# Kernel optimization log

Measured on AMD Instinct MI355X. Metric: run time of the kernel, lower is better.

Reference implementation:

```python
import jax, jax.numpy as jnp
import numpy as np

B, S, E = 4, 2048, 512
Q, FFN = 8, 2048


def setup_inputs() -> dict:
    key = jax.random.key(0)
    k_x, k_th, k_w1, k_w2 = jax.random.split(key, 4)
    x = jax.random.normal(k_x, (B, S, E), dtype=jnp.float32)
    # trainable RY angles, one per wire
    theta = jax.random.normal(k_th, (Q,), dtype=jnp.float32)
    W1 = jax.random.normal(k_w1, (Q, FFN), dtype=jnp.float32) / np.sqrt(Q)
    b1 = jnp.zeros((FFN,), dtype=jnp.float32)
    W2 = jax.random.normal(k_w2, (FFN, E), dtype=jnp.float32) / np.sqrt(FFN)
    b2 = jnp.zeros((E,), dtype=jnp.float32)
    return {"x": x, "theta": theta, "W1": W1, "b1": b1, "W2": W2, "b2": b2}


def reference(x, theta, W1, b1, W2, b2):
    # Quantum circuit: |0> -> RX(x_i) -> RY(theta_i) -> <Z> per wire.
    # No entangling gates, so the 8-qubit state factorizes; simulate each
    # qubit's 2 complex amplitudes, batched over all tokens & wires at once.
    n_wires = theta.shape[0]
    xq = x[..., :n_wires]                     # encoder uses input_idx 0..7: [B,S,Q]
    # RX(x)|0> = cos(x/2)|0> - i sin(x/2)|1>
    a = jnp.cos(xq * 0.5).astype(jnp.complex64)
    b = (-1j) * jnp.sin(xq * 0.5).astype(jnp.complex64)
    # RY(theta) = [[c,-s],[s,c]], c=cos(theta/2), s=sin(theta/2)
    c = jnp.cos(theta * 0.5).astype(jnp.complex64)
    s = jnp.sin(theta * 0.5).astype(jnp.complex64)
    a2 = c * a - s * b
    b2_ = s * a + c * b
    # <Z> = |amp0|^2 - |amp1|^2  -> [B,S,Q]
    z = (jnp.abs(a2) ** 2 - jnp.abs(b2_) ** 2).astype(x.dtype)
    # dropout is identity at inference
    h = jax.nn.relu(jnp.einsum('bsq,qf->bsf', z, W1) + b1)
    return jnp.einsum('bsf,fe->bse', h, W2) + b2
```

## Files before the change

### kernel.cpp

```cpp
#include <hip/hip_runtime.h>
#include <hip/hip_bf16.h>

typedef __bf16 bf16_t;
typedef __bf16 bf16x4 __attribute__((ext_vector_type(4)));
typedef __bf16 bf16x8 __attribute__((ext_vector_type(8)));
typedef float f32x4 __attribute__((ext_vector_type(4)));

#define M_TOT 8192
#define N_TOT 512
#define K_TOT 2048
#define E_TOT 512

typedef const __attribute__((address_space(1))) void* gas_ptr;
typedef __attribute__((address_space(3))) void* las_ptr;

__device__ __forceinline__ void gload_lds16(const void* g, void* l) {
    __builtin_amdgcn_global_load_lds((gas_ptr)g, (las_ptr)l, 16, 0, 0);
}

__device__ __forceinline__ bf16x8 zero8() {
    bf16x8 v;
#pragma unroll
    for (int i = 0; i < 8; ++i) v[i] = (bf16_t)0.0f;
    return v;
}

__global__ __launch_bounds__(256)
void prep3_kernel(const float* __restrict__ x,
                  const float* __restrict__ theta,
                  const float* __restrict__ W1,
                  const float* __restrict__ b1,
                  const float* __restrict__ W2,
                  bf16_t* __restrict__ W2t,
                  bf16_t* __restrict__ zb,
                  bf16_t* __restrict__ W1t)
{
    const int b = blockIdx.x;
    if (b < 256) {
        __shared__ bf16_t T[64][66];
        const int k0 = (b >> 3) * 64;
        const int n0 = (b & 7) * 64;
        const int kl = threadIdx.x >> 4;
        const int n4 = threadIdx.x & 15;
#pragma unroll
        for (int i = 0; i < 4; ++i) {
            int k = kl + i * 16;
            float4 v = *(const float4*)(W2 + (size_t)(k0 + k) * N_TOT + n0 + n4 * 4);
            T[n4 * 4 + 0][k] = (bf16_t)v.x;
            T[n4 * 4 + 1][k] = (bf16_t)v.y;
            T[n4 * 4 + 2][k] = (bf16_t)v.z;
            T[n4 * 4 + 3][k] = (bf16_t)v.w;
        }
        __syncthreads();
        const int nl = threadIdx.x >> 4;
        const int k4 = threadIdx.x & 15;
#pragma unroll
        for (int i = 0; i < 4; ++i) {
            int n = nl + i * 16;
            bf16x4 v;
            v[0] = T[n][k4 * 4 + 0];
            v[1] = T[n][k4 * 4 + 1];
            v[2] = T[n][k4 * 4 + 2];
            v[3] = T[n][k4 * 4 + 3];
            *(bf16x4*)(W2t + (size_t)(n0 + n) * K_TOT + k0 + k4 * 4) = v;
        }
    } else if (b < 288) {
        const int m = (b - 256) * 256 + threadIdx.x;
        float4 x0 = *(const float4*)(x + (size_t)m * E_TOT);
        float4 x1 = *(const float4*)(x + (size_t)m * E_TOT + 4);
        float xs[8] = {x0.x, x0.y, x0.z, x0.w, x1.x, x1.y, x1.z, x1.w};
        bf16x8 lo;
#pragma unroll
        for (int q = 0; q < 8; ++q)
            lo[q] = (bf16_t)(__builtin_cosf(theta[q]) * __builtin_cosf(xs[q]));
        bf16x8 hi = zero8();
        hi[0] = (bf16_t)1.0f;
        *(bf16x8*)(zb + (size_t)m * 16)     = lo;
        *(bf16x8*)(zb + (size_t)m * 16 + 8) = hi;
    } else {
        const int f = (b - 288) * 256 + threadIdx.x;
        bf16x8 lo;
#pragma unroll
        for (int q = 0; q < 8; ++q)
            lo[q] = (bf16_t)W1[(size_t)q * K_TOT + f];
        bf16x8 hi = zero8();
        hi[0] = (bf16_t)b1[f];
        *(bf16x8*)(W1t + (size_t)f * 16)     = lo;
        *(bf16x8*)(W1t + (size_t)f * 16 + 8) = hi;
    }
}

__global__ __launch_bounds__(256, 2)
void ffq_gemm_kernel(const bf16_t* __restrict__ zb,
                     const bf16_t* __restrict__ W1t,
                     const bf16_t* __restrict__ W2t,
                     const float* __restrict__ b2,
                     float* __restrict__ out)
{
    __shared__ bf16_t Alds[64 * 64];
    __shared__ bf16_t Blds[128 * 64];

    const int t = threadIdx.x;
    const int w = t >> 6, l = t & 63;
    const int m_base = blockIdx.y * 64;
    const int n_base = blockIdx.x * 128;
    const int wm = w >> 1, wn = w & 1;
    const int l15 = l & 15, lq = l >> 4;
    const int lrow = l >> 3, lseg = l & 7;

    bf16x8 zfrag = zero8();
    if (lq < 2)
        zfrag = *(const bf16x8*)(zb + (size_t)(m_base + w * 16 + l15) * 16 + lq * 8);

    f32x4 acc[2][4];
#pragma unroll
    for (int mt = 0; mt < 2; ++mt)
#pragma unroll
        for (int nt = 0; nt < 4; ++nt)
            acc[mt][nt] = (f32x4){0.f, 0.f, 0.f, 0.f};

    for (int k0 = 0; k0 < K_TOT; k0 += 64) {
        bf16x8 wf[4];
#pragma unroll
        for (int ft = 0; ft < 4; ++ft) wf[ft] = zero8();
        if (lq < 2) {
#pragma unroll
            for (int ft = 0; ft < 4; ++ft)
                wf[ft] = *(const bf16x8*)(W1t + (size_t)(k0 + ft * 16 + l15) * 16 + lq * 8);
        }

#pragma unroll
        for (int j = 0; j < 4; ++j) {
            int n = j * 32 + w * 8 + lrow;
            int g = lseg ^ (n & 7);
            gload_lds16(W2t + (size_t)(n_base + n) * K_TOT + k0 + g * 8,
                        (bf16_t*)Blds + j * 2048 + w * 512);
        }

        const int m_loc = w * 16 + l15;
#pragma unroll
        for (int ft = 0; ft < 4; ++ft) {
            f32x4 hacc = (f32x4){0.f, 0.f, 0.f, 0.f};
            hacc = __builtin_amdgcn_mfma_f32_16x16x32_bf16(wf[ft], zfrag, hacc, 0, 0, 0);
            bf16x4 hv;
#pragma unroll
            for (int r = 0; r < 4; ++r) hv[r] = (bf16_t)fmaxf(hacc[r], 0.f);
            int fseg = ft * 2 + (lq >> 1);
            int slot = fseg ^ (m_loc & 7);
            *(bf16x4*)(Alds + m_loc * 64 + slot * 8 + (lq & 1) * 4) = hv;
        }

        __syncthreads();

#pragma unroll
        for (int kk = 0; kk < 2; ++kk) {
            bf16x8 af[2], bfr[4];
#pragma unroll
            for (int mt = 0; mt < 2; ++mt) {
                int r = wm * 32 + mt * 16 + l15;
                int s = (kk * 4 + lq) ^ (r & 7);
                af[mt] = *(const bf16x8*)(Alds + r * 64 + s * 8);
            }
#pragma unroll
            for (int nt = 0; nt < 4; ++nt) {
                int r = wn * 64 + nt * 16 + l15;
                int s = (kk * 4 + lq) ^ (r & 7);
                bfr[nt] = *(const bf16x8*)(Blds + r * 64 + s * 8);
            }
#pragma unroll
            for (int mt = 0; mt < 2; ++mt)
#pragma unroll
                for (int nt = 0; nt < 4; ++nt)
                    acc[mt][nt] = __builtin_amdgcn_mfma_f32_16x16x32_bf16(
                        af[mt], bfr[nt], acc[mt][nt], 0, 0, 0);
        }
        __syncthreads();
    }

#pragma unroll
    for (int nt = 0; nt < 4; ++nt) {
        int col = n_base + wn * 64 + nt * 16 + l15;
        float bias = b2[col];
#pragma unroll
        for (int mt = 0; mt < 2; ++mt) {
#pragma unroll
            for (int r = 0; r < 4; ++r) {
                int row = m_base + wm * 32 + mt * 16 + lq * 4 + r;
                out[(size_t)row * N_TOT + col] = acc[mt][nt][r] + bias;
            }
        }
    }
}

extern "C" void kernel_launch(void* const* d_in, const int* in_sizes, int n_in,
                              void* d_out, int out_size, void* d_ws, size_t ws_size,
                              hipStream_t stream) {
    const float* x     = (const float*)d_in[0];
    const float* theta = (const float*)d_in[1];
    const float* W1    = (const float*)d_in[2];
    const float* b1    = (const float*)d_in[3];
    const float* W2    = (const float*)d_in[4];
    const float* b2    = (const float*)d_in[5];
    float* out = (float*)d_out;

    const size_t W2T_BYTES = (size_t)N_TOT * K_TOT * sizeof(bf16_t);
    const size_t ZB_BYTES  = (size_t)M_TOT * 16 * sizeof(bf16_t);

    bf16_t* W2t = (bf16_t*)d_ws;
    bf16_t* zb  = (bf16_t*)((char*)d_ws + W2T_BYTES);
    bf16_t* W1t = (bf16_t*)((char*)d_ws + W2T_BYTES + ZB_BYTES);

    prep3_kernel<<<296, 256, 0, stream>>>(x, theta, W1, b1, W2, W2t, zb, W1t);

    dim3 grid(N_TOT / 128, M_TOT / 64);
    ffq_gemm_kernel<<<grid, 256, 0, stream>>>(zb, W1t, W2t, b2, out);
}
```

Before: 114.5 us.

## Double-buffer LDS stages and grow the fused FFN tile to 128x128

Each block now covers a 128x128 output tile instead of 64x128, so every block recomputes fewer H rows per output and loads fewer W2 tiles. LDS holds two A/B buffer pairs, so staging the next K-step and computing its relu(zW1) tile overlap with the MFMAs of the current step. This leaves one barrier per step. The grid halves to 256 blocks and each thread holds twice as many accumulators, which lowers occupancy and may increase register pressure.

```diff
diff --git a/kernel.cpp b/kernel.cpp
--- a/kernel.cpp
+++ b/kernel.cpp
@@ -10,6 +10,7 @@
 #define N_TOT 512
 #define K_TOT 2048
 #define E_TOT 512
+#define NT    (K_TOT / 64)
 
 typedef const __attribute__((address_space(1))) void* gas_ptr;
 typedef __attribute__((address_space(3))) void* las_ptr;
@@ -90,91 +91,130 @@
     }
 }
 
-__global__ __launch_bounds__(256, 2)
+__device__ __forceinline__ void load_wf(const bf16_t* __restrict__ W1t, int k0,
+                                        int l15, int lq, bf16x8 wf[4]) {
+#pragma unroll
+    for (int ft = 0; ft < 4; ++ft) wf[ft] = zero8();
+    if (lq < 2) {
+#pragma unroll
+        for (int ft = 0; ft < 4; ++ft)
+            wf[ft] = *(const bf16x8*)(W1t + (size_t)(k0 + ft * 16 + l15) * 16 + lq * 8);
+    }
+}
+
+__device__ __forceinline__ void stage_B(const bf16_t* __restrict__ W2t, int n_base,
+                                        int k0, bf16_t* Bb, int w, int lrow, int lseg) {
+#pragma unroll
+    for (int j = 0; j < 4; ++j) {
+        int n = j * 32 + w * 8 + lrow;
+        int g = lseg ^ (n & 7);
+        gload_lds16(W2t + (size_t)(n_base + n) * K_TOT + k0 + g * 8,
+                    Bb + j * 2048 + w * 512);
+    }
+}
+
+__device__ __forceinline__ void h_stage(const bf16x8 wf[4], const bf16x8 zfrag[2],
+                                        bf16_t* Ab, int w, int l15, int lq) {
+#pragma unroll
+    for (int mh = 0; mh < 2; ++mh) {
+        int m_loc = w * 32 + mh * 16 + l15;
+#pragma unroll
+        for (int ft = 0; ft < 4; ++ft) {
+            f32x4 hacc = (f32x4){0.f, 0.f, 0.f, 0.f};
+            hacc = __builtin_amdgcn_mfma_f32_16x16x32_bf16(wf[ft], zfrag[mh], hacc, 0, 0, 0);
+            bf16x4 hv;
+#pragma unroll
+            for (int r = 0; r < 4; ++r) hv[r] = (bf16_t)fmaxf(hacc[r], 0.f);
+            int fseg = ft * 2 + (lq >> 1);
+            int slot = fseg ^ (m_loc & 7);
+            *(bf16x4*)(Ab + m_loc * 64 + slot * 8 + (lq & 1) * 4) = hv;
+        }
+    }
+}
+
+__device__ __forceinline__ void main_mfma(const bf16_t* Ab, const bf16_t* Bb,
+                                          int wm, int wn, int l15, int lq,
+                                          f32x4 acc[4][4]) {
+#pragma unroll
+    for (int kk = 0; kk < 2; ++kk) {
+        bf16x8 af[4], bfr[4];
+#pragma unroll
+        for (int mt = 0; mt < 4; ++mt) {
+            int r = wm * 64 + mt * 16 + l15;
+            int s = (kk * 4 + lq) ^ (r & 7);
+            af[mt] = *(const bf16x8*)(Ab + r * 64 + s * 8);
+        }
+#pragma unroll
+        for (int nt = 0; nt < 4; ++nt) {
+            int r = wn * 64 + nt * 16 + l15;
+            int s = (kk * 4 + lq) ^ (r & 7);
+            bfr[nt] = *(const bf16x8*)(Bb + r * 64 + s * 8);
+        }
+#pragma unroll
+        for (int mt = 0; mt < 4; ++mt)
+#pragma unroll
+            for (int nt = 0; nt < 4; ++nt)
+                acc[mt][nt] = __builtin_amdgcn_mfma_f32_16x16x32_bf16(
+                    af[mt], bfr[nt], acc[mt][nt], 0, 0, 0);
+    }
+}
+
+__global__ __launch_bounds__(256)
 void ffq_gemm_kernel(const bf16_t* __restrict__ zb,
                      const bf16_t* __restrict__ W1t,
                      const bf16_t* __restrict__ W2t,
                      const float* __restrict__ b2,
                      float* __restrict__ out)
 {
-    __shared__ bf16_t Alds[64 * 64];
-    __shared__ bf16_t Blds[128 * 64];
+    __shared__ bf16_t Alds[2][128 * 64];
+    __shared__ bf16_t Blds[2][128 * 64];
 
     const int t = threadIdx.x;
     const int w = t >> 6, l = t & 63;
-    const int m_base = blockIdx.y * 64;
+    const int m_base = blockIdx.y * 128;
     const int n_base = blockIdx.x * 128;
     const int wm = w >> 1, wn = w & 1;
     const int l15 = l & 15, lq = l >> 4;
     const int lrow = l >> 3, lseg = l & 7;
 
-    bf16x8 zfrag = zero8();
-    if (lq < 2)
-        zfrag = *(const bf16x8*)(zb + (size_t)(m_base + w * 16 + l15) * 16 + lq * 8);
-
-    f32x4 acc[2][4];
-#pragma unroll
-    for (int mt = 0; mt < 2; ++mt)
+    bf16x8 zfrag[2];
+#pragma unroll
+    for (int mh = 0; mh < 2; ++mh) {
+        zfrag[mh] = zero8();
+        if (lq < 2)
+            zfrag[mh] = *(const bf16x8*)(zb + (size_t)(m_base + w * 32 + mh * 16 + l15) * 16 + lq * 8);
+    }
+
+    f32x4 acc[4][4];
+#pragma unroll
+    for (int mt = 0; mt < 4; ++mt)
 #pragma unroll
         for (int nt = 0; nt < 4; ++nt)
             acc[mt][nt] = (f32x4){0.f, 0.f, 0.f, 0.f};
 
-    for (int k0 = 0; k0 < K_TOT; k0 += 64) {
-        bf16x8 wf[4];
-#pragma unroll
-        for (int ft = 0; ft < 4; ++ft) wf[ft] = zero8();
-        if (lq < 2) {
-#pragma unroll
-            for (int ft = 0; ft < 4; ++ft)
-                wf[ft] = *(const bf16x8*)(W1t + (size_t)(k0 + ft * 16 + l15) * 16 + lq * 8);
-        }
-
-#pragma unroll
-        for (int j = 0; j < 4; ++j) {
-            int n = j * 32 + w * 8 + lrow;
-            int g = lseg ^ (n & 7);
-            gload_lds16(W2t + (size_t)(n_base + n) * K_TOT + k0 + g * 8,
-                        (bf16_t*)Blds + j * 2048 + w * 512);
-        }
-
-        const int m_loc = w * 16 + l15;
-#pragma unroll
-        for (int ft = 0; ft < 4; ++ft) {
-            f32x4 hacc = (f32x4){0.f, 0.f, 0.f, 0.f};
-            hacc = __builtin_amdgcn_mfma_f32_16x16x32_bf16(wf[ft], zfrag, hacc, 0, 0, 0);
-            bf16x4 hv;
-#pragma unroll
-            for (int r = 0; r < 4; ++r) hv[r] = (bf16_t)fmaxf(hacc[r], 0.f);
-            int fseg = ft * 2 + (lq >> 1);
-            int slot = fseg ^ (m_loc & 7);
-            *(bf16x4*)(Alds + m_loc * 64 + slot * 8 + (lq & 1) * 4) = hv;
-        }
-
+    {
+        bf16x8 wf0[4];
+        load_wf(W1t, 0, l15, lq, wf0);
+        stage_B(W2t, n_base, 0, Blds[0], w, lrow, lseg);
+        h_stage(wf0, zfrag, Alds[0], w, l15, lq);
+    }
+
+    for (int it = 0; it < NT; it += 2) {
+        bf16x8 wfa[4];
+        load_wf(W1t, (it + 1) * 64, l15, lq, wfa);
         __syncthreads();
-
-#pragma unroll
-        for (int kk = 0; kk < 2; ++kk) {
-            bf16x8 af[2], bfr[4];
-#pragma unroll
-            for (int mt = 0; mt < 2; ++mt) {
-                int r = wm * 32 + mt * 16 + l15;
-                int s = (kk * 4 + lq) ^ (r & 7);
-                af[mt] = *(const bf16x8*)(Alds + r * 64 + s * 8);
-            }
-#pragma unroll
-            for (int nt = 0; nt < 4; ++nt) {
-                int r = wn * 64 + nt * 16 + l15;
-                int s = (kk * 4 + lq) ^ (r & 7);
-                bfr[nt] = *(const bf16x8*)(Blds + r * 64 + s * 8);
-            }
-#pragma unroll
-            for (int mt = 0; mt < 2; ++mt)
-#pragma unroll
-                for (int nt = 0; nt < 4; ++nt)
-                    acc[mt][nt] = __builtin_amdgcn_mfma_f32_16x16x32_bf16(
-                        af[mt], bfr[nt], acc[mt][nt], 0, 0, 0);
-        }
+        stage_B(W2t, n_base, (it + 1) * 64, Blds[1], w, lrow, lseg);
+        h_stage(wfa, zfrag, Alds[1], w, l15, lq);
+        main_mfma(Alds[0], Blds[0], wm, wn, l15, lq, acc);
+
+        bf16x8 wfb[4];
+        if (it + 2 < NT) load_wf(W1t, (it + 2) * 64, l15, lq, wfb);
         __syncthreads();
+        if (it + 2 < NT) {
+            stage_B(W2t, n_base, (it + 2) * 64, Blds[0], w, lrow, lseg);
+            h_stage(wfb, zfrag, Alds[0], w, l15, lq);
+        }
+        main_mfma(Alds[1], Blds[1], wm, wn, l15, lq, acc);
     }
 
 #pragma unroll
@@ -182,10 +222,10 @@
         int col = n_base + wn * 64 + nt * 16 + l15;
         float bias = b2[col];
 #pragma unroll
-        for (int mt = 0; mt < 2; ++mt) {
+        for (int mt = 0; mt < 4; ++mt) {
 #pragma unroll
             for (int r = 0; r < 4; ++r) {
-                int row = m_base + wm * 32 + mt * 16 + lq * 4 + r;
+                int row = m_base + wm * 64 + mt * 16 + lq * 4 + r;
                 out[(size_t)row * N_TOT + col] = acc[mt][nt][r] + bias;
             }
         }
@@ -212,6 +252,6 @@
 
     prep3_kernel<<<296, 256, 0, stream>>>(x, theta, W1, b1, W2, W2t, zb, W1t);
 
-    dim3 grid(N_TOT / 128, M_TOT / 64);
+    dim3 grid(N_TOT / 128, M_TOT / 128);
     ffq_gemm_kernel<<<grid, 256, 0, stream>>>(zb, W1t, W2t, b2, out);
 }
```

After: 120.3 us. 1.05x slower.

## Keep hidden activations in registers and double-buffer W2 tiles in LDS

Applied to the files above, without the earlier changes.

The W1 rows are now stored in a permuted order, so the first MFMA's output lanes map directly onto A-operand fragments for the second GEMM. This removes the LDS round trip for the ReLU hidden tile. W2 tiles are double-buffered in LDS through register staging, with the next tile's global load issued before the current tile's compute. Blocks grow to 512 threads covering a 128x128 output tile, which recomputes the hidden values per wave and raises register pressure.

```diff
diff --git a/kernel.cpp b/kernel.cpp
--- a/kernel.cpp
+++ b/kernel.cpp
@@ -10,13 +10,7 @@
 #define N_TOT 512
 #define K_TOT 2048
 #define E_TOT 512
-
-typedef const __attribute__((address_space(1))) void* gas_ptr;
-typedef __attribute__((address_space(3))) void* las_ptr;
-
-__device__ __forceinline__ void gload_lds16(const void* g, void* l) {
-    __builtin_amdgcn_global_load_lds((gas_ptr)g, (las_ptr)l, 16, 0, 0);
-}
+#define NT    32
 
 __device__ __forceinline__ bf16x8 zero8() {
     bf16x8 v;
@@ -26,14 +20,14 @@
 }
 
 __global__ __launch_bounds__(256)
-void prep3_kernel(const float* __restrict__ x,
+void prep4_kernel(const float* __restrict__ x,
                   const float* __restrict__ theta,
                   const float* __restrict__ W1,
                   const float* __restrict__ b1,
                   const float* __restrict__ W2,
                   bf16_t* __restrict__ W2t,
                   bf16_t* __restrict__ zb,
-                  bf16_t* __restrict__ W1t)
+                  bf16_t* __restrict__ W1p)
 {
     const int b = blockIdx.x;
     if (b < 256) {
@@ -78,39 +72,118 @@
         *(bf16x8*)(zb + (size_t)m * 16)     = lo;
         *(bf16x8*)(zb + (size_t)m * 16 + 8) = hi;
     } else {
-        const int f = (b - 288) * 256 + threadIdx.x;
+        const int d  = (b - 288) * 256 + threadIdx.x;
+        const int c  = d >> 5;
+        const int dd = d & 31;
+        const int p  = dd >> 4;
+        const int rr = dd & 15;
+        const int f  = c * 32 + ((rr >> 2) << 3) + (p << 2) + (rr & 3);
         bf16x8 lo;
 #pragma unroll
         for (int q = 0; q < 8; ++q)
             lo[q] = (bf16_t)W1[(size_t)q * K_TOT + f];
         bf16x8 hi = zero8();
         hi[0] = (bf16_t)b1[f];
-        *(bf16x8*)(W1t + (size_t)f * 16)     = lo;
-        *(bf16x8*)(W1t + (size_t)f * 16 + 8) = hi;
-    }
-}
-
-__global__ __launch_bounds__(256, 2)
+        *(bf16x8*)(W1p + (size_t)d * 16)     = lo;
+        *(bf16x8*)(W1p + (size_t)d * 16 + 8) = hi;
+    }
+}
+
+__device__ __forceinline__ void load_B(const bf16_t* __restrict__ W2t, int n_base,
+                                       int k0, int t, uint4 gv[2]) {
+#pragma unroll
+    for (int j = 0; j < 2; ++j) {
+        int s = t + j * 512;
+        int n = s >> 3;
+        int g = (s & 7) ^ (n & 7);
+        gv[j] = *(const uint4*)(W2t + (size_t)(n_base + n) * K_TOT + k0 + g * 8);
+    }
+}
+__device__ __forceinline__ void write_B(bf16_t* Bb, int t, const uint4 gv[2]) {
+#pragma unroll
+    for (int j = 0; j < 2; ++j) {
+        int s = t + j * 512;
+        *(uint4*)(Bb + (s >> 3) * 64 + (s & 7) * 8) = gv[j];
+    }
+}
+
+__device__ __forceinline__ void load_wf(const bf16_t* __restrict__ W1p, int k0,
+                                        int l15, int lq, bf16x8 wf[4]) {
+#pragma unroll
+    for (int i = 0; i < 4; ++i) wf[i] = zero8();
+    if (lq < 2) {
+        const int base = (k0 >> 5) * 2;
+#pragma unroll
+        for (int i = 0; i < 4; ++i)
+            wf[i] = *(const bf16x8*)(W1p + (size_t)((base + i) * 16 + l15) * 16 + lq * 8);
+    }
+}
+
+__device__ __forceinline__ void compute_tile(const bf16_t* Bb, const bf16x8 wf[4],
+                                             const bf16x8 zfrag[2],
+                                             int wn, int l15, int lq,
+                                             f32x4 acc[2][4]) {
+    bf16x8 bfr[2][4];
+#pragma unroll
+    for (int c = 0; c < 2; ++c)
+#pragma unroll
+        for (int nt = 0; nt < 4; ++nt) {
+            int r = wn * 64 + nt * 16 + l15;
+            int s = (c * 4 + lq) ^ (r & 7);
+            bfr[c][nt] = *(const bf16x8*)(Bb + r * 64 + s * 8);
+        }
+
+    bf16x8 af[2][2];
+#pragma unroll
+    for (int mt = 0; mt < 2; ++mt)
+#pragma unroll
+        for (int c = 0; c < 2; ++c) {
+            f32x4 h0 = (f32x4){0.f, 0.f, 0.f, 0.f};
+            f32x4 h1 = (f32x4){0.f, 0.f, 0.f, 0.f};
+            h0 = __builtin_amdgcn_mfma_f32_16x16x32_bf16(wf[c * 2 + 0], zfrag[mt], h0, 0, 0, 0);
+            h1 = __builtin_amdgcn_mfma_f32_16x16x32_bf16(wf[c * 2 + 1], zfrag[mt], h1, 0, 0, 0);
+            bf16x8 a;
+#pragma unroll
+            for (int r = 0; r < 4; ++r) {
+                a[r]     = (bf16_t)fmaxf(h0[r], 0.f);
+                a[r + 4] = (bf16_t)fmaxf(h1[r], 0.f);
+            }
+            af[mt][c] = a;
+        }
+
+#pragma unroll
+    for (int c = 0; c < 2; ++c)
+#pragma unroll
+        for (int mt = 0; mt < 2; ++mt)
+#pragma unroll
+            for (int nt = 0; nt < 4; ++nt)
+                acc[mt][nt] = __builtin_amdgcn_mfma_f32_16x16x32_bf16(
+                    af[mt][c], bfr[c][nt], acc[mt][nt], 0, 0, 0);
+}
+
+__global__ __launch_bounds__(512, 2)
 void ffq_gemm_kernel(const bf16_t* __restrict__ zb,
-                     const bf16_t* __restrict__ W1t,
+                     const bf16_t* __restrict__ W1p,
                      const bf16_t* __restrict__ W2t,
                      const float* __restrict__ b2,
                      float* __restrict__ out)
 {
-    __shared__ bf16_t Alds[64 * 64];
-    __shared__ bf16_t Blds[128 * 64];
+    __shared__ bf16_t Blds[2][128 * 64];
 
     const int t = threadIdx.x;
     const int w = t >> 6, l = t & 63;
-    const int m_base = blockIdx.y * 64;
+    const int m_base = blockIdx.y * 128;
     const int n_base = blockIdx.x * 128;
     const int wm = w >> 1, wn = w & 1;
     const int l15 = l & 15, lq = l >> 4;
-    const int lrow = l >> 3, lseg = l & 7;
-
-    bf16x8 zfrag = zero8();
-    if (lq < 2)
-        zfrag = *(const bf16x8*)(zb + (size_t)(m_base + w * 16 + l15) * 16 + lq * 8);
+
+    bf16x8 zfrag[2];
+#pragma unroll
+    for (int mt = 0; mt < 2; ++mt) {
+        zfrag[mt] = zero8();
+        if (lq < 2)
+            zfrag[mt] = *(const bf16x8*)(zb + (size_t)(m_base + wm * 32 + mt * 16 + l15) * 16 + lq * 8);
+    }
 
     f32x4 acc[2][4];
 #pragma unroll
@@ -119,62 +192,28 @@
         for (int nt = 0; nt < 4; ++nt)
             acc[mt][nt] = (f32x4){0.f, 0.f, 0.f, 0.f};
 
-    for (int k0 = 0; k0 < K_TOT; k0 += 64) {
-        bf16x8 wf[4];
-#pragma unroll
-        for (int ft = 0; ft < 4; ++ft) wf[ft] = zero8();
-        if (lq < 2) {
-#pragma unroll
-            for (int ft = 0; ft < 4; ++ft)
-                wf[ft] = *(const bf16x8*)(W1t + (size_t)(k0 + ft * 16 + l15) * 16 + lq * 8);
-        }
-
-#pragma unroll
-        for (int j = 0; j < 4; ++j) {
-            int n = j * 32 + w * 8 + lrow;
-            int g = lseg ^ (n & 7);
-            gload_lds16(W2t + (size_t)(n_base + n) * K_TOT + k0 + g * 8,
-                        (bf16_t*)Blds + j * 2048 + w * 512);
-        }
-
-        const int m_loc = w * 16 + l15;
-#pragma unroll
-        for (int ft = 0; ft < 4; ++ft) {
-            f32x4 hacc = (f32x4){0.f, 0.f, 0.f, 0.f};
-            hacc = __builtin_amdgcn_mfma_f32_16x16x32_bf16(wf[ft], zfrag, hacc, 0, 0, 0);
-            bf16x4 hv;
-#pragma unroll
-            for (int r = 0; r < 4; ++r) hv[r] = (bf16_t)fmaxf(hacc[r], 0.f);
-            int fseg = ft * 2 + (lq >> 1);
-            int slot = fseg ^ (m_loc & 7);
-            *(bf16x4*)(Alds + m_loc * 64 + slot * 8 + (lq & 1) * 4) = hv;
-        }
-
+    uint4 gv[2];
+    bf16x8 wfA[4], wfB[4];
+
+    load_B(W2t, n_base, 0, t, gv);
+    load_wf(W1p, 0, l15, lq, wfA);
+    write_B(Blds[0], t, gv);
+
+    for (int it = 0; it < NT; it += 2) {
         __syncthreads();
-
-#pragma unroll
-        for (int kk = 0; kk < 2; ++kk) {
-            bf16x8 af[2], bfr[4];
-#pragma unroll
-            for (int mt = 0; mt < 2; ++mt) {
-                int r = wm * 32 + mt * 16 + l15;
-                int s = (kk * 4 + lq) ^ (r & 7);
-                af[mt] = *(const bf16x8*)(Alds + r * 64 + s * 8);
-            }
-#pragma unroll
-            for (int nt = 0; nt < 4; ++nt) {
-                int r = wn * 64 + nt * 16 + l15;
-                int s = (kk * 4 + lq) ^ (r & 7);
-                bfr[nt] = *(const bf16x8*)(Blds + r * 64 + s * 8);
-            }
-#pragma unroll
-            for (int mt = 0; mt < 2; ++mt)
-#pragma unroll
-                for (int nt = 0; nt < 4; ++nt)
-                    acc[mt][nt] = __builtin_amdgcn_mfma_f32_16x16x32_bf16(
-                        af[mt], bfr[nt], acc[mt][nt], 0, 0, 0);
-        }
+        load_B(W2t, n_base, (it + 1) * 64, t, gv);
+        load_wf(W1p, (it + 1) * 64, l15, lq, wfB);
+        compute_tile(Blds[0], wfA, zfrag, wn, l15, lq, acc);
+        write_B(Blds[1], t, gv);
+
         __syncthreads();
+        const bool more = (it + 2 < NT);
+        if (more) {
+            load_B(W2t, n_base, (it + 2) * 64, t, gv);
+            load_wf(W1p, (it + 2) * 64, l15, lq, wfA);
+        }
+        compute_tile(Blds[1], wfB, zfrag, wn, l15, lq, acc);
+        if (more) write_B(Blds[0], t, gv);
     }
 
 #pragma unroll
@@ -208,10 +247,10 @@
 
     bf16_t* W2t = (bf16_t*)d_ws;
     bf16_t* zb  = (bf16_t*)((char*)d_ws + W2T_BYTES);
-    bf16_t* W1t = (bf16_t*)((char*)d_ws + W2T_BYTES + ZB_BYTES);
-
-    prep3_kernel<<<296, 256, 0, stream>>>(x, theta, W1, b1, W2, W2t, zb, W1t);
-
-    dim3 grid(N_TOT / 128, M_TOT / 64);
-    ffq_gemm_kernel<<<grid, 256, 0, stream>>>(zb, W1t, W2t, b2, out);
-}
+    bf16_t* W1p = (bf16_t*)((char*)d_ws + W2T_BYTES + ZB_BYTES);
+
+    prep4_kernel<<<296, 256, 0, stream>>>(x, theta, W1, b1, W2, W2t, zb, W1p);
+
+    dim3 grid(N_TOT / 128, M_TOT / 128);
+    ffq_gemm_kernel<<<grid, 512, 0, stream>>>(zb, W1p, W2t, b2, out);
+}
```

Result: slower. 128.2 us (+12.0%).
